# Optimization experiments

Hardware: AMD Instinct MI355X
Metric: run time of the kernel (lower is better)

Reference implementation:

```python
import jax, jax.numpy as jnp
import numpy as np

D = 128
N0, N1, N2 = 1048576, 131072, 8192   # node counts per sampled layer (src->tgt)
E0, E1 = 1048576, 131072             # edges per layer


def setup_inputs() -> dict:
    key = jax.random.key(0)
    ks = jax.random.split(key, 11)
    s = 1.0 / np.sqrt(D)  # torch Linear init scale
    u = lambda k: jax.random.uniform(k, (D, D), jnp.float32, -s, s)
    return {
        "x": jax.random.normal(ks[0], (N0, D), jnp.float32),
        "Wl0": u(ks[1]), "bl0": jnp.zeros((D,), jnp.float32), "Wr0": u(ks[2]),
        "Wl1": u(ks[3]), "bl1": jnp.zeros((D,), jnp.float32), "Wr1": u(ks[4]),
        "src0": jax.random.randint(ks[5], (E0,), 0, N0, jnp.int32),
        "dst0": jax.random.randint(ks[6], (E0,), 0, N1, jnp.int32),
        "src1": jax.random.randint(ks[7], (E1,), 0, N1, jnp.int32),
        "dst1": jax.random.randint(ks[8], (E1,), 0, N2, jnp.int32),
    }


def _sage_conv(x_src, x_tgt, src, dst, Wl, bl, Wr, n_tgt):
    # message: gather source features along edges; aggregate: mean per target
    msg = x_src[src]                                        # [E, D]
    agg = jax.ops.segment_sum(msg, dst, num_segments=n_tgt)  # [n_tgt, D]
    cnt = jax.ops.segment_sum(jnp.ones((src.shape[0], 1), x_src.dtype),
                              dst, num_segments=n_tgt)       # [n_tgt, 1]
    mean = agg / jnp.maximum(cnt, 1.0)                      # zero-degree -> 0
    return mean @ Wl + bl + x_tgt @ Wr


def reference(x, Wl0, bl0, Wr0, Wl1, bl1, Wr1, src0, dst0, src1, dst1):
    # layer 0: N0 sources -> N1 targets
    h = _sage_conv(x, x[:N1], src0, dst0, Wl0, bl0, Wr0, N1)
    h = jax.nn.relu(h)  # dropout p=0.0 is identity
    # layer 1: N1 sources -> N2 targets
    h = _sage_conv(h, h[:N2], src1, dst1, Wl1, bl1, Wr1, N2)
    return jax.nn.relu(h)
```

## Files before the change

kernel.cpp:

```cpp
#include <hip/hip_runtime.h>
#include <hip/hip_bf16.h>

#define D 128
#define N0_ 1048576
#define N1_ 131072
#define N2_ 8192
#define E0_ 1048576
#define E1_ 131072

typedef float f32x4 __attribute__((ext_vector_type(4)));
typedef short bf16x8 __attribute__((ext_vector_type(8)));

__device__ __forceinline__ short f2bf(float f) {
    __hip_bfloat16 h = __float2bfloat16(f);
    return __builtin_bit_cast(short, h);
}
__device__ __forceinline__ float bf2f(short s) {
    return __bfloat162float(__builtin_bit_cast(__hip_bfloat16, s));
}

__global__ __launch_bounds__(256) void zero_kernel(int4* __restrict__ p, int n4) {
    int i = blockIdx.x * 256 + threadIdx.x;
    if (i < n4) p[i] = int4{0, 0, 0, 0};
}

__global__ __launch_bounds__(256) void hist_kernel(const int* __restrict__ dst,
                                                   int* __restrict__ deg, int nE) {
    int e = blockIdx.x * 256 + threadIdx.x;
    if (e < nE) atomicAdd(&deg[dst[e]], 1);
}

__global__ __launch_bounds__(256) void scan1(const int* __restrict__ deg,
                                             int* __restrict__ offs,
                                             int* __restrict__ bsum, int n) {
    __shared__ int ws[4];
    int i = blockIdx.x * 256 + threadIdx.x;
    int lane = threadIdx.x & 63, wid = threadIdx.x >> 6;
    int v = (i < n) ? deg[i] : 0;
    int incl = v;
#pragma unroll
    for (int d = 1; d < 64; d <<= 1) {
        int u = __shfl_up(incl, d);
        if (lane >= d) incl += u;
    }
    if (lane == 63) ws[wid] = incl;
    __syncthreads();
    if (threadIdx.x == 0) {
        int a = 0;
        for (int w = 0; w < 4; ++w) { int t = ws[w]; ws[w] = a; a += t; }
        bsum[blockIdx.x] = a;
    }
    __syncthreads();
    if (i < n) offs[i] = incl - v + ws[wid];
}

__global__ __launch_bounds__(512) void scan2(int* __restrict__ bsum, int nb) {
    __shared__ int ws[8];
    int i = threadIdx.x, lane = i & 63, wid = i >> 6;
    int v = (i < nb) ? bsum[i] : 0;
    int incl = v;
#pragma unroll
    for (int d = 1; d < 64; d <<= 1) {
        int u = __shfl_up(incl, d);
        if (lane >= d) incl += u;
    }
    if (lane == 63) ws[wid] = incl;
    __syncthreads();
    if (i == 0) {
        int a = 0;
        for (int w = 0; w < 8; ++w) { int t = ws[w]; ws[w] = a; a += t; }
    }
    __syncthreads();
    if (i < nb) bsum[i] = incl - v + ws[wid];
}

__global__ __launch_bounds__(256) void scan3(int* __restrict__ offs,
                                             const int* __restrict__ bsum,
                                             int* __restrict__ cur, int n) {
    int i = blockIdx.x * 256 + threadIdx.x;
    if (i < n) {
        int o = offs[i] + bsum[blockIdx.x];
        offs[i] = o;
        cur[i] = o;
    }
}

__global__ __launch_bounds__(256) void scatter_edges(const int* __restrict__ src,
                                                     const int* __restrict__ dst,
                                                     int* __restrict__ cur,
                                                     int* __restrict__ eidx, int nE) {
    int e = blockIdx.x * 256 + threadIdx.x;
    if (e < nE) {
        int pos = atomicAdd(&cur[dst[e]], 1);
        eidx[pos] = src[e];
    }
}

template <bool SRCBF16>
__device__ __forceinline__ float2 row_load(const void* xsrc_v, int s, int lane) {
    if (SRCBF16) {
        const short* xs = (const short*)xsrc_v;
        ushort2 v = ((const ushort2*)(xs + (size_t)s * D))[lane];
        return float2{bf2f((short)v.x), bf2f((short)v.y)};
    } else {
        const float* xs = (const float*)xsrc_v;
        return ((const float2*)(xs + (size_t)s * D))[lane];
    }
}

template <bool SRCBF16>
__global__ __launch_bounds__(256) void aggregate(const void* __restrict__ xsrc_v,
                                                 const int* __restrict__ eidx,
                                                 const int* __restrict__ offs,
                                                 const int* __restrict__ deg,
                                                 short* __restrict__ mean, int ntgt) {
    const int lane = threadIdx.x & 63;
    const int gw = (blockIdx.x * 256 + threadIdx.x) >> 6;
    const int nw = (gridDim.x * 256) >> 6;
    for (int t = gw; t < ntgt; t += nw) {
        const int start = offs[t], d = deg[t];
        float ax = 0.0f, ay = 0.0f;
        for (int base = 0; base < d; base += 64) {
            const int nc = min(64, d - base);
            int sidx = (lane < nc) ? eidx[start + base + lane] : 0;
            int i = 0;
            for (; i + 8 <= nc; i += 8) {
                float2 v[8];
#pragma unroll
                for (int u = 0; u < 8; ++u) {
                    int s = __shfl(sidx, i + u);
                    v[u] = row_load<SRCBF16>(xsrc_v, s, lane);
                }
#pragma unroll
                for (int u = 0; u < 8; ++u) { ax += v[u].x; ay += v[u].y; }
            }
            for (; i + 4 <= nc; i += 4) {
                float2 v[4];
#pragma unroll
                for (int u = 0; u < 4; ++u) {
                    int s = __shfl(sidx, i + u);
                    v[u] = row_load<SRCBF16>(xsrc_v, s, lane);
                }
#pragma unroll
                for (int u = 0; u < 4; ++u) { ax += v[u].x; ay += v[u].y; }
            }
            for (; i < nc; ++i) {
                int s = __shfl(sidx, i);
                float2 v = row_load<SRCBF16>(xsrc_v, s, lane);
                ax += v.x;
                ay += v.y;
            }
        }
        const float r = (d > 0) ? 1.0f / (float)d : 0.0f;
        ushort2 o;
        o.x = (unsigned short)f2bf(ax * r);
        o.y = (unsigned short)f2bf(ay * r);
        ((ushort2*)(mean + (size_t)t * D))[lane] = o;
    }
}

template <bool XBF16, bool OUTBF16>
__global__ __launch_bounds__(256) void sage_update(
    const short* __restrict__ mean, const void* __restrict__ xtgt_v,
    const float* __restrict__ Wl, const float* __restrict__ Wr,
    const float* __restrict__ bl, void* __restrict__ out_v, int ntiles) {
    __shared__ __align__(16) char wt[128 * 256 * 2];

    {
        int t = threadIdx.x;
        int j = t & 127;
        int half = t >> 7;
        const float* W = half ? Wr : Wl;
        for (int k = 0; k < 128; ++k) {
            float v = W[k * 128 + j];
            int kk = half * 128 + k;
            int byte = (j * 512 + kk * 2) ^ ((j & 7) << 4);
            *reinterpret_cast<short*>(wt + byte) = f2bf(v);
        }
    }
    __syncthreads();

    const int wave = threadIdx.x >> 6, lane = threadIdx.x & 63;
    const int rl = lane & 15;
    const int kq = lane >> 4;

    float blv[8];
#pragma unroll
    for (int nt = 0; nt < 8; ++nt) blv[nt] = bl[nt * 16 + rl];

    for (int tile = blockIdx.x; tile < ntiles; tile += gridDim.x) {
        const int grow = tile * 64 + wave * 16 + rl;
        f32x4 acc[8] = {};

#pragma unroll
        for (int ks = 0; ks < 8; ++ks) {
            const int k0 = ks * 32 + kq * 8;
            bf16x8 af;
            if (ks < 4) {
                af = *reinterpret_cast<const bf16x8*>(mean + (size_t)grow * D + k0);
            } else {
                const int kx = k0 - 128;
                if (XBF16) {
                    af = *reinterpret_cast<const bf16x8*>(
                        (const short*)xtgt_v + (size_t)grow * D + kx);
                } else {
                    const float4* p = reinterpret_cast<const float4*>(
                        (const float*)xtgt_v + (size_t)grow * D + kx);
                    float4 a = p[0], b = p[1];
                    af[0] = f2bf(a.x); af[1] = f2bf(a.y);
                    af[2] = f2bf(a.z); af[3] = f2bf(a.w);
                    af[4] = f2bf(b.x); af[5] = f2bf(b.y);
                    af[6] = f2bf(b.z); af[7] = f2bf(b.w);
                }
            }
#pragma unroll
            for (int nt = 0; nt < 8; ++nt) {
                const int j = nt * 16 + rl;
                const int byte = (j * 512 + k0 * 2) ^ ((j & 7) << 4);
                bf16x8 bfr = *reinterpret_cast<const bf16x8*>(wt + byte);
                acc[nt] =
                    __builtin_amdgcn_mfma_f32_16x16x32_bf16(af, bfr, acc[nt], 0, 0, 0);
            }
        }

        const int orow_base = tile * 64 + wave * 16 + kq * 4;
#pragma unroll
        for (int nt = 0; nt < 8; ++nt) {
            const int col = nt * 16 + rl;
#pragma unroll
            for (int r = 0; r < 4; ++r) {
                float v = acc[nt][r] + blv[nt];
                v = fmaxf(v, 0.0f);
                const size_t idx = (size_t)(orow_base + r) * D + col;
                if (OUTBF16)
                    ((short*)out_v)[idx] = f2bf(v);
                else
                    ((float*)out_v)[idx] = v;
            }
        }
    }
}

extern "C" void kernel_launch(void* const* d_in, const int* in_sizes, int n_in,
                              void* d_out, int out_size, void* d_ws, size_t ws_size,
                              hipStream_t stream) {
    const float* x   = (const float*)d_in[0];
    const float* Wl0 = (const float*)d_in[1];
    const float* bl0 = (const float*)d_in[2];
    const float* Wr0 = (const float*)d_in[3];
    const float* Wl1 = (const float*)d_in[4];
    const float* bl1 = (const float*)d_in[5];
    const float* Wr1 = (const float*)d_in[6];
    const int* src0  = (const int*)d_in[7];
    const int* dst0  = (const int*)d_in[8];
    const int* src1  = (const int*)d_in[9];
    const int* dst1  = (const int*)d_in[10];

    char* ws = (char*)d_ws;
    int*   deg0  = (int*)(ws);
    int*   deg1  = (int*)(ws + 524288);
    int*   cur0  = (int*)(ws + 557056);
    int*   cur1  = (int*)(ws + 1081344);
    int*   bsum  = (int*)(ws + 1114112);
    int*   offs0 = (int*)(ws + 1118208);
    int*   offs1 = (int*)(ws + 1642496);
    int*   eidx0 = (int*)(ws + 1675264);
    int*   eidx1 = (int*)(ws + 5869568);
    short* mean0 = (short*)(ws + 6393856);
    short* mean1 = (short*)(ws + 39948288);
    short* h     = (short*)(ws + 42045440);

    zero_kernel<<<136, 256, 0, stream>>>((int4*)ws, 34816);

    hist_kernel<<<E0_ / 256, 256, 0, stream>>>(dst0, deg0, E0_);
    scan1<<<N1_ / 256, 256, 0, stream>>>(deg0, offs0, bsum, N1_);
    scan2<<<1, 512, 0, stream>>>(bsum, N1_ / 256);
    scan3<<<N1_ / 256, 256, 0, stream>>>(offs0, bsum, cur0, N1_);
    scatter_edges<<<E0_ / 256, 256, 0, stream>>>(src0, dst0, cur0, eidx0, E0_);
    aggregate<false><<<4096, 256, 0, stream>>>(x, eidx0, offs0, deg0, mean0, N1_);
    sage_update<false, true><<<1024, 256, 0, stream>>>(
        mean0, x, Wl0, Wr0, bl0, h, N1_ / 64);

    hist_kernel<<<E1_ / 256, 256, 0, stream>>>(dst1, deg1, E1_);
    scan1<<<N2_ / 256, 256, 0, stream>>>(deg1, offs1, bsum, N2_);
    scan2<<<1, 512, 0, stream>>>(bsum, N2_ / 256);
    scan3<<<N2_ / 256, 256, 0, stream>>>(offs1, bsum, cur1, N2_);
    scatter_edges<<<E1_ / 256, 256, 0, stream>>>(src1, dst1, cur1, eidx1, E1_);
    aggregate<true><<<2048, 256, 0, stream>>>(h, eidx1, offs1, deg1, mean1, N2_);
    sage_update<true, false><<<128, 256, 0, stream>>>(
        mean1, h, Wl1, Wr1, bl1, d_out, N2_ / 64);
}
```

Before: 324.1 us.

## Fuse aggregation into update GEMM and merge both layers' CSR build

Aggregation now runs inside the update kernel: each block gathers the mean rows for its 64 targets into a swizzled LDS tile and feeds them straight to the MFMA, so the mean buffer is never written to or read back from global memory. The histogram, scan and scatter stages for both layers are merged into single launches over a joint degree array with int4-vectorized edge reads. The end offset produced by the scatter atomics doubles as the CSR pointer, which removes the separate cursor array. This cuts launches and global traffic, but each block now stages its weights without overlap and the grid is fixed at one 64-row tile per block.

```diff
diff --git a/kernel.cpp b/kernel.cpp
--- a/kernel.cpp
+++ b/kernel.cpp
@@ -24,10 +24,23 @@
     if (i < n4) p[i] = int4{0, 0, 0, 0};
 }
 
-__global__ __launch_bounds__(256) void hist_kernel(const int* __restrict__ dst,
-                                                   int* __restrict__ deg, int nE) {
-    int e = blockIdx.x * 256 + threadIdx.x;
-    if (e < nE) atomicAdd(&deg[dst[e]], 1);
+__global__ __launch_bounds__(256) void hist_both(const int* __restrict__ dst0,
+                                                 const int* __restrict__ dst1,
+                                                 int* __restrict__ deg) {
+    int g = blockIdx.x * 256 + threadIdx.x;
+    if (g < E0_ / 4) {
+        int4 d4 = ((const int4*)dst0)[g];
+        atomicAdd(&deg[d4.x], 1);
+        atomicAdd(&deg[d4.y], 1);
+        atomicAdd(&deg[d4.z], 1);
+        atomicAdd(&deg[d4.w], 1);
+    } else {
+        int4 d4 = ((const int4*)dst1)[g - E0_ / 4];
+        atomicAdd(&deg[N1_ + d4.x], 1);
+        atomicAdd(&deg[N1_ + d4.y], 1);
+        atomicAdd(&deg[N1_ + d4.z], 1);
+        atomicAdd(&deg[N1_ + d4.w], 1);
+    }
 }
 
 __global__ __launch_bounds__(256) void scan1(const int* __restrict__ deg,
@@ -54,8 +67,8 @@
     if (i < n) offs[i] = incl - v + ws[wid];
 }
 
-__global__ __launch_bounds__(512) void scan2(int* __restrict__ bsum, int nb) {
-    __shared__ int ws[8];
+__global__ __launch_bounds__(1024) void scan2(int* __restrict__ bsum, int nb) {
+    __shared__ int ws[16];
     int i = threadIdx.x, lane = i & 63, wid = i >> 6;
     int v = (i < nb) ? bsum[i] : 0;
     int incl = v;
@@ -68,31 +81,43 @@
     __syncthreads();
     if (i == 0) {
         int a = 0;
-        for (int w = 0; w < 8; ++w) { int t = ws[w]; ws[w] = a; a += t; }
+        for (int w = 0; w < 16; ++w) { int t = ws[w]; ws[w] = a; a += t; }
     }
     __syncthreads();
     if (i < nb) bsum[i] = incl - v + ws[wid];
 }
 
 __global__ __launch_bounds__(256) void scan3(int* __restrict__ offs,
-                                             const int* __restrict__ bsum,
-                                             int* __restrict__ cur, int n) {
+                                             const int* __restrict__ bsum, int n) {
     int i = blockIdx.x * 256 + threadIdx.x;
-    if (i < n) {
-        int o = offs[i] + bsum[blockIdx.x];
-        offs[i] = o;
-        cur[i] = o;
-    }
-}
-
-__global__ __launch_bounds__(256) void scatter_edges(const int* __restrict__ src,
-                                                     const int* __restrict__ dst,
-                                                     int* __restrict__ cur,
-                                                     int* __restrict__ eidx, int nE) {
-    int e = blockIdx.x * 256 + threadIdx.x;
-    if (e < nE) {
-        int pos = atomicAdd(&cur[dst[e]], 1);
-        eidx[pos] = src[e];
+    if (i < n) offs[i] += bsum[blockIdx.x];
+}
+
+__global__ __launch_bounds__(256) void scatter_both(const int* __restrict__ src0,
+                                                    const int* __restrict__ dst0,
+                                                    const int* __restrict__ src1,
+                                                    const int* __restrict__ dst1,
+                                                    int* __restrict__ offs,
+                                                    int* __restrict__ eidx0,
+                                                    int* __restrict__ eidx1) {
+    int g = blockIdx.x * 256 + threadIdx.x;
+    if (g < E0_ / 4) {
+        int4 s4 = ((const int4*)src0)[g];
+        int4 d4 = ((const int4*)dst0)[g];
+        int p;
+        p = atomicAdd(&offs[d4.x], 1); eidx0[p] = s4.x;
+        p = atomicAdd(&offs[d4.y], 1); eidx0[p] = s4.y;
+        p = atomicAdd(&offs[d4.z], 1); eidx0[p] = s4.z;
+        p = atomicAdd(&offs[d4.w], 1); eidx0[p] = s4.w;
+    } else {
+        int gq = g - E0_ / 4;
+        int4 s4 = ((const int4*)src1)[gq];
+        int4 d4 = ((const int4*)dst1)[gq];
+        int p;
+        p = atomicAdd(&offs[N1_ + d4.x], 1); eidx1[p - E0_] = s4.x;
+        p = atomicAdd(&offs[N1_ + d4.y], 1); eidx1[p - E0_] = s4.y;
+        p = atomicAdd(&offs[N1_ + d4.z], 1); eidx1[p - E0_] = s4.z;
+        p = atomicAdd(&offs[N1_ + d4.w], 1); eidx1[p - E0_] = s4.w;
     }
 }
 
@@ -108,63 +133,17 @@
     }
 }
 
-template <bool SRCBF16>
-__global__ __launch_bounds__(256) void aggregate(const void* __restrict__ xsrc_v,
-                                                 const int* __restrict__ eidx,
-                                                 const int* __restrict__ offs,
-                                                 const int* __restrict__ deg,
-                                                 short* __restrict__ mean, int ntgt) {
-    const int lane = threadIdx.x & 63;
-    const int gw = (blockIdx.x * 256 + threadIdx.x) >> 6;
-    const int nw = (gridDim.x * 256) >> 6;
-    for (int t = gw; t < ntgt; t += nw) {
-        const int start = offs[t], d = deg[t];
-        float ax = 0.0f, ay = 0.0f;
-        for (int base = 0; base < d; base += 64) {
-            const int nc = min(64, d - base);
-            int sidx = (lane < nc) ? eidx[start + base + lane] : 0;
-            int i = 0;
-            for (; i + 8 <= nc; i += 8) {
-                float2 v[8];
-#pragma unroll
-                for (int u = 0; u < 8; ++u) {
-                    int s = __shfl(sidx, i + u);
-                    v[u] = row_load<SRCBF16>(xsrc_v, s, lane);
-                }
-#pragma unroll
-                for (int u = 0; u < 8; ++u) { ax += v[u].x; ay += v[u].y; }
-            }
-            for (; i + 4 <= nc; i += 4) {
-                float2 v[4];
-#pragma unroll
-                for (int u = 0; u < 4; ++u) {
-                    int s = __shfl(sidx, i + u);
-                    v[u] = row_load<SRCBF16>(xsrc_v, s, lane);
-                }
-#pragma unroll
-                for (int u = 0; u < 4; ++u) { ax += v[u].x; ay += v[u].y; }
-            }
-            for (; i < nc; ++i) {
-                int s = __shfl(sidx, i);
-                float2 v = row_load<SRCBF16>(xsrc_v, s, lane);
-                ax += v.x;
-                ay += v.y;
-            }
-        }
-        const float r = (d > 0) ? 1.0f / (float)d : 0.0f;
-        ushort2 o;
-        o.x = (unsigned short)f2bf(ax * r);
-        o.y = (unsigned short)f2bf(ay * r);
-        ((ushort2*)(mean + (size_t)t * D))[lane] = o;
-    }
-}
-
-template <bool XBF16, bool OUTBF16>
-__global__ __launch_bounds__(256) void sage_update(
-    const short* __restrict__ mean, const void* __restrict__ xtgt_v,
-    const float* __restrict__ Wl, const float* __restrict__ Wr,
-    const float* __restrict__ bl, void* __restrict__ out_v, int ntiles) {
+template <bool SRCBF16, bool OUTBF16>
+__global__ __launch_bounds__(256) void agg_update(
+    const void* __restrict__ xsrc_v, const int* __restrict__ eidx,
+    const int* __restrict__ offs_end, const int* __restrict__ deg,
+    int joint_base, int eidx_sub, const float* __restrict__ Wl,
+    const float* __restrict__ Wr, const float* __restrict__ bl,
+    void* __restrict__ out_v) {
     __shared__ __align__(16) char wt[128 * 256 * 2];
+    __shared__ __align__(16) char mt[64 * 256];
+
+    const int wave = threadIdx.x >> 6, lane = threadIdx.x & 63;
 
     {
         int t = threadIdx.x;
@@ -178,9 +157,54 @@
             *reinterpret_cast<short*>(wt + byte) = f2bf(v);
         }
     }
-    __syncthreads();
-
-    const int wave = threadIdx.x >> 6, lane = threadIdx.x & 63;
+
+    for (int tt = 0; tt < 16; ++tt) {
+        const int tl = wave * 16 + tt;
+        const int tj = joint_base + blockIdx.x * 64 + tl;
+        const int dgr = deg[tj];
+        const int start = offs_end[tj] - dgr - eidx_sub;
+        float ax = 0.0f, ay = 0.0f;
+        for (int base = 0; base < dgr; base += 64) {
+            const int nc = min(64, dgr - base);
+            int sidx = (lane < nc) ? eidx[start + base + lane] : 0;
+            int i = 0;
+            for (; i + 8 <= nc; i += 8) {
+                float2 v[8];
+#pragma unroll
+                for (int u = 0; u < 8; ++u) {
+                    int s = __shfl(sidx, i + u);
+                    v[u] = row_load<SRCBF16>(xsrc_v, s, lane);
+                }
+#pragma unroll
+                for (int u = 0; u < 8; ++u) { ax += v[u].x; ay += v[u].y; }
+            }
+            for (; i + 4 <= nc; i += 4) {
+                float2 v[4];
+#pragma unroll
+                for (int u = 0; u < 4; ++u) {
+                    int s = __shfl(sidx, i + u);
+                    v[u] = row_load<SRCBF16>(xsrc_v, s, lane);
+                }
+#pragma unroll
+                for (int u = 0; u < 4; ++u) { ax += v[u].x; ay += v[u].y; }
+            }
+            for (; i < nc; ++i) {
+                int s = __shfl(sidx, i);
+                float2 v = row_load<SRCBF16>(xsrc_v, s, lane);
+                ax += v.x;
+                ay += v.y;
+            }
+        }
+        const float r = (dgr > 0) ? 1.0f / (float)dgr : 0.0f;
+        ushort2 o;
+        o.x = (unsigned short)f2bf(ax * r);
+        o.y = (unsigned short)f2bf(ay * r);
+        const int byte = (tl * 256 + lane * 4) ^ ((tl & 7) << 4);
+        *reinterpret_cast<ushort2*>(mt + byte) = o;
+    }
+
+    __syncthreads();
+
     const int rl = lane & 15;
     const int kq = lane >> 4;
 
@@ -188,55 +212,55 @@
 #pragma unroll
     for (int nt = 0; nt < 8; ++nt) blv[nt] = bl[nt * 16 + rl];
 
-    for (int tile = blockIdx.x; tile < ntiles; tile += gridDim.x) {
-        const int grow = tile * 64 + wave * 16 + rl;
-        f32x4 acc[8] = {};
-
-#pragma unroll
-        for (int ks = 0; ks < 8; ++ks) {
-            const int k0 = ks * 32 + kq * 8;
-            bf16x8 af;
-            if (ks < 4) {
-                af = *reinterpret_cast<const bf16x8*>(mean + (size_t)grow * D + k0);
+    const int grow = blockIdx.x * 64 + wave * 16 + rl;
+    const int rowl = wave * 16 + rl;
+    f32x4 acc[8] = {};
+
+#pragma unroll
+    for (int ks = 0; ks < 8; ++ks) {
+        const int k0 = ks * 32 + kq * 8;
+        bf16x8 af;
+        if (ks < 4) {
+            const int byte = (rowl * 256 + k0 * 2) ^ ((rowl & 7) << 4);
+            af = *reinterpret_cast<const bf16x8*>(mt + byte);
+        } else {
+            const int kx = k0 - 128;
+            if (SRCBF16) {
+                af = *reinterpret_cast<const bf16x8*>(
+                    (const short*)xsrc_v + (size_t)grow * D + kx);
             } else {
-                const int kx = k0 - 128;
-                if (XBF16) {
-                    af = *reinterpret_cast<const bf16x8*>(
-                        (const short*)xtgt_v + (size_t)grow * D + kx);
-                } else {
-                    const float4* p = reinterpret_cast<const float4*>(
-                        (const float*)xtgt_v + (size_t)grow * D + kx);
-                    float4 a = p[0], b = p[1];
-                    af[0] = f2bf(a.x); af[1] = f2bf(a.y);
-                    af[2] = f2bf(a.z); af[3] = f2bf(a.w);
-                    af[4] = f2bf(b.x); af[5] = f2bf(b.y);
-                    af[6] = f2bf(b.z); af[7] = f2bf(b.w);
-                }
+                const float4* p = reinterpret_cast<const float4*>(
+                    (const float*)xsrc_v + (size_t)grow * D + kx);
+                float4 a = p[0], b = p[1];
+                af[0] = f2bf(a.x); af[1] = f2bf(a.y);
+                af[2] = f2bf(a.z); af[3] = f2bf(a.w);
+                af[4] = f2bf(b.x); af[5] = f2bf(b.y);
+                af[6] = f2bf(b.z); af[7] = f2bf(b.w);
             }
-#pragma unroll
-            for (int nt = 0; nt < 8; ++nt) {
-                const int j = nt * 16 + rl;
-                const int byte = (j * 512 + k0 * 2) ^ ((j & 7) << 4);
-                bf16x8 bfr = *reinterpret_cast<const bf16x8*>(wt + byte);
-                acc[nt] =
-                    __builtin_amdgcn_mfma_f32_16x16x32_bf16(af, bfr, acc[nt], 0, 0, 0);
-            }
-        }
-
-        const int orow_base = tile * 64 + wave * 16 + kq * 4;
+        }
 #pragma unroll
         for (int nt = 0; nt < 8; ++nt) {
-            const int col = nt * 16 + rl;
-#pragma unroll
-            for (int r = 0; r < 4; ++r) {
-                float v = acc[nt][r] + blv[nt];
-                v = fmaxf(v, 0.0f);
-                const size_t idx = (size_t)(orow_base + r) * D + col;
-                if (OUTBF16)
-                    ((short*)out_v)[idx] = f2bf(v);
-                else
-                    ((float*)out_v)[idx] = v;
-            }
+            const int j = nt * 16 + rl;
+            const int byte = (j * 512 + k0 * 2) ^ ((j & 7) << 4);
+            bf16x8 bfr = *reinterpret_cast<const bf16x8*>(wt + byte);
+            acc[nt] =
+                __builtin_amdgcn_mfma_f32_16x16x32_bf16(af, bfr, acc[nt], 0, 0, 0);
+        }
+    }
+
+    const int orow_base = blockIdx.x * 64 + wave * 16 + kq * 4;
+#pragma unroll
+    for (int nt = 0; nt < 8; ++nt) {
+        const int col = nt * 16 + rl;
+#pragma unroll
+        for (int r = 0; r < 4; ++r) {
+            float v = acc[nt][r] + blv[nt];
+            v = fmaxf(v, 0.0f);
+            const size_t idx = (size_t)(orow_base + r) * D + col;
+            if (OUTBF16)
+                ((short*)out_v)[idx] = f2bf(v);
+            else
+                ((float*)out_v)[idx] = v;
         }
     }
 }
@@ -257,36 +281,24 @@
     const int* dst1  = (const int*)d_in[10];
 
     char* ws = (char*)d_ws;
-    int*   deg0  = (int*)(ws);
-    int*   deg1  = (int*)(ws + 524288);
-    int*   cur0  = (int*)(ws + 557056);
-    int*   cur1  = (int*)(ws + 1081344);
+    int*   deg   = (int*)(ws);
+    int*   offs  = (int*)(ws + 557056);
     int*   bsum  = (int*)(ws + 1114112);
-    int*   offs0 = (int*)(ws + 1118208);
-    int*   offs1 = (int*)(ws + 1642496);
-    int*   eidx0 = (int*)(ws + 1675264);
-    int*   eidx1 = (int*)(ws + 5869568);
-    short* mean0 = (short*)(ws + 6393856);
-    short* mean1 = (short*)(ws + 39948288);
-    short* h     = (short*)(ws + 42045440);
-
-    zero_kernel<<<136, 256, 0, stream>>>((int4*)ws, 34816);
-
-    hist_kernel<<<E0_ / 256, 256, 0, stream>>>(dst0, deg0, E0_);
-    scan1<<<N1_ / 256, 256, 0, stream>>>(deg0, offs0, bsum, N1_);
-    scan2<<<1, 512, 0, stream>>>(bsum, N1_ / 256);
-    scan3<<<N1_ / 256, 256, 0, stream>>>(offs0, bsum, cur0, N1_);
-    scatter_edges<<<E0_ / 256, 256, 0, stream>>>(src0, dst0, cur0, eidx0, E0_);
-    aggregate<false><<<4096, 256, 0, stream>>>(x, eidx0, offs0, deg0, mean0, N1_);
-    sage_update<false, true><<<1024, 256, 0, stream>>>(
-        mean0, x, Wl0, Wr0, bl0, h, N1_ / 64);
-
-    hist_kernel<<<E1_ / 256, 256, 0, stream>>>(dst1, deg1, E1_);
-    scan1<<<N2_ / 256, 256, 0, stream>>>(deg1, offs1, bsum, N2_);
-    scan2<<<1, 512, 0, stream>>>(bsum, N2_ / 256);
-    scan3<<<N2_ / 256, 256, 0, stream>>>(offs1, bsum, cur1, N2_);
-    scatter_edges<<<E1_ / 256, 256, 0, stream>>>(src1, dst1, cur1, eidx1, E1_);
-    aggregate<true><<<2048, 256, 0, stream>>>(h, eidx1, offs1, deg1, mean1, N2_);
-    sage_update<true, false><<<128, 256, 0, stream>>>(
-        mean1, h, Wl1, Wr1, bl1, d_out, N2_ / 64);
-}
+    int*   eidx0 = (int*)(ws + 1118208);
+    int*   eidx1 = (int*)(ws + 5312512);
+    short* h     = (short*)(ws + 5836800);
+
+    const int NJ = N1_ + N2_;
+
+    zero_kernel<<<136, 256, 0, stream>>>((int4*)deg, NJ / 4);
+    hist_both<<<(E0_ + E1_) / 1024, 256, 0, stream>>>(dst0, dst1, deg);
+    scan1<<<NJ / 256, 256, 0, stream>>>(deg, offs, bsum, NJ);
+    scan2<<<1, 1024, 0, stream>>>(bsum, NJ / 256);
+    scan3<<<NJ / 256, 256, 0, stream>>>(offs, bsum, NJ);
+    scatter_both<<<(E0_ + E1_) / 1024, 256, 0, stream>>>(src0, dst0, src1, dst1,
+                                                         offs, eidx0, eidx1);
+    agg_update<false, true><<<N1_ / 64, 256, 0, stream>>>(
+        x, eidx0, offs, deg, 0, 0, Wl0, Wr0, bl0, h);
+    agg_update<true, false><<<N2_ / 64, 256, 0, stream>>>(
+        h, eidx1, offs, deg, N1_, E0_, Wl1, Wr1, bl1, d_out);
+}
```

Measured after the change: 415.6 us. 28.2% more time.
